# Kernel tuning notes

Hardware: AMD Instinct MI355X
Metric: run time of the kernel (lower is better)

Reference implementation:

```python
import jax, jax.numpy as jnp
import numpy as np
from jax import lax

SOFTPLUS_THRESHOLD = 20.0

def _softplus_thresh(z):
    # softplus(z, beta=1, threshold=20): linear above threshold
    return jnp.where(z > SOFTPLUS_THRESHOLD, z,
                     jnp.log1p(jnp.exp(jnp.minimum(z, SOFTPLUS_THRESHOLD))))

def setup_inputs() -> dict:
    key = jax.random.key(0)
    ks = jax.random.split(key, 8)
    L, E, R, N = 512, 5120, 160, 16
    scale = 0.02
    x = jax.random.normal(ks[0], (1, 1, L, E), dtype=jnp.float32)
    W_dt_low = jax.random.normal(ks[1], (E, R), dtype=jnp.float32) * scale
    W_dt = jax.random.normal(ks[2], (R, E), dtype=jnp.float32) * scale
    dt_bias = jax.random.normal(ks[3], (E,), dtype=jnp.float32) * scale
    W_B = jax.random.normal(ks[4], (E, N), dtype=jnp.float32) * scale
    W_C = jax.random.normal(ks[5], (E, N), dtype=jnp.float32) * scale
    # A_log ~ log of positive values so A = -exp(A_log) is a stable decay
    A_log = jnp.log(1.0 + jax.random.uniform(ks[6], (E, N), dtype=jnp.float32) * 15.0)
    D = jax.random.normal(ks[7], (E,), dtype=jnp.float32)
    return {"x": x, "W_dt_low": W_dt_low, "W_dt": W_dt, "dt_bias": dt_bias,
            "W_B": W_B, "W_C": W_C, "A_log": A_log, "D": D}

def reference(x, W_dt_low, W_dt, dt_bias, W_B, W_C, A_log, D):
    orig_shape = x.shape              # [1,1,L,E]
    L, E = orig_shape[-2], orig_shape[-1]
    xf = x.reshape(L, E)
    # delta_t: x -> dt_rank -> d_inner, then thresholded softplus
    delta = _softplus_thresh((xf @ W_dt_low) @ W_dt + dt_bias)   # [L,E]
    A = -jnp.exp(A_log)                                          # [E,N]
    # discretization: abar = exp(delta * A), bbar = delta * B * x
    abar = jnp.exp(delta[:, :, None] * A[None])                  # [L,E,N]
    B = xf @ W_B                                                 # [L,N]
    bbar = delta[:, :, None] * B[:, None, :] * xf[:, :, None]    # [L,E,N]
    # linear recurrence h_t = abar_t * h_{t-1} + bbar_t via associative scan
    def combine(c1, c2):
        a1, b1 = c1
        a2, b2 = c2
        return a1 * a2, a2 * b1 + b2
    _, h = lax.associative_scan(combine, (abar, bbar), axis=0)   # [L,E,N]
    C = xf @ W_C                                                 # [L,N]
    y = jnp.einsum('len,ln->le', h, C)                           # hc_sum_reduce
    out = xf * D + y
    return out.reshape(orig_shape)
```

## Files before the change

kernel.cpp:

```cpp
#include <hip/hip_runtime.h>
#include <math.h>

#define LL 512
#define EE 5120
#define RR 160
#define NS 16
#define NTOT 192
#define KS 32
#define KCHUNK 160
#define CH 8
#define NC 64

#define XCONV_BLOCKS 1280
#define WALL_TILES   960
#define WDT_TILES    800

typedef __attribute__((ext_vector_type(8))) short short8;
typedef __attribute__((ext_vector_type(4))) short short4v;
typedef __attribute__((ext_vector_type(4))) float f32x4;

__device__ inline float softplus_t(float z) {
    return z > 20.f ? z : log1pf(__expf(fminf(z, 20.f)));
}

__device__ inline short f2bf(float f) {
    unsigned u = __float_as_uint(f);
    unsigned r = (u + 0x7FFFu + ((u >> 16) & 1u)) >> 16;
    return (short)r;
}

__device__ inline float bf2f(unsigned short u) {
    return __uint_as_float(((unsigned)u) << 16);
}

__global__ __launch_bounds__(256) void prep_kernel(
        const float* __restrict__ x,
        const float* __restrict__ Wlow,
        const float* __restrict__ WB,
        const float* __restrict__ WC,
        const float* __restrict__ Wdt,
        short* __restrict__ xb,
        short* __restrict__ WallT,
        short* __restrict__ WdtT) {
    const int tid = threadIdx.x;
    const int bid = blockIdx.x;
    if (bid < XCONV_BLOCKS) {
        size_t base = (size_t)bid * 2048 + (size_t)tid * 8;
        float4 v0 = *reinterpret_cast<const float4*>(x + base);
        float4 v1 = *reinterpret_cast<const float4*>(x + base + 4);
        short8 o;
        o[0] = f2bf(v0.x); o[1] = f2bf(v0.y); o[2] = f2bf(v0.z); o[3] = f2bf(v0.w);
        o[4] = f2bf(v1.x); o[5] = f2bf(v1.y); o[6] = f2bf(v1.z); o[7] = f2bf(v1.w);
        *reinterpret_cast<short8*>(xb + base) = o;
        return;
    }
    __shared__ float tile[32][33];
    const int row = tid >> 3, col4 = (tid & 7) * 4;
    if (bid < XCONV_BLOCKS + WALL_TILES) {
        const int t = bid - XCONV_BLOCKS;
        const int k0 = (t / 6) * 32, n0 = (t % 6) * 32;
#pragma unroll
        for (int i = 0; i < 4; ++i) {
            int n = n0 + col4 + i, k = k0 + row;
            float v;
            if (n < RR)            v = Wlow[(size_t)k * RR + n];
            else if (n < RR + NS)  v = WB[(size_t)k * NS + (n - RR)];
            else                   v = WC[(size_t)k * NS + (n - RR - NS)];
            tile[row][col4 + i] = v;
        }
        __syncthreads();
        const int nr = tid >> 3, kc = (tid & 7) * 4;
        short4v o;
#pragma unroll
        for (int i = 0; i < 4; ++i) o[i] = f2bf(tile[kc + i][nr]);
        *reinterpret_cast<short4v*>(WallT + (size_t)(n0 + nr) * EE + k0 + kc) = o;
    } else {
        const int t = bid - XCONV_BLOCKS - WALL_TILES;
        const int n0 = (t / 5) * 32, k0 = (t % 5) * 32;
#pragma unroll
        for (int i = 0; i < 4; ++i)
            tile[row][col4 + i] = Wdt[(size_t)(k0 + row) * EE + n0 + col4 + i];
        __syncthreads();
        const int nr = tid >> 3, kc = (tid & 7) * 4;
        short4v o;
#pragma unroll
        for (int i = 0; i < 4; ++i) o[i] = f2bf(tile[kc + i][nr]);
        *reinterpret_cast<short4v*>(WdtT + (size_t)(n0 + nr) * RR + k0 + kc) = o;
    }
}

__global__ __launch_bounds__(256) void g1m_kernel(
        const short* __restrict__ xb,
        const short* __restrict__ WallT,
        short* __restrict__ part) {
    const int tid = threadIdx.x;
    const int w = tid >> 6, l = tid & 63;
    const int wm = w >> 1, wn = w & 1;
    const int m0 = blockIdx.x * 64 + wm * 32;
    const int n0 = blockIdx.y * 64 + wn * 32;
    const int kz = blockIdx.z;
    const int row16 = l & 15, kg = (l >> 4) * 8;
    f32x4 acc[2][2] = {};
    const short* ap0 = xb + (size_t)(m0 + row16) * EE + kz * KCHUNK + kg;
    const short* ap1 = ap0 + (size_t)16 * EE;
    const short* bp0 = WallT + (size_t)(n0 + row16) * EE + kz * KCHUNK + kg;
    const short* bp1 = bp0 + (size_t)16 * EE;
#pragma unroll
    for (int s = 0; s < KCHUNK / 32; ++s) {
        short8 a0 = *reinterpret_cast<const short8*>(ap0 + s * 32);
        short8 a1 = *reinterpret_cast<const short8*>(ap1 + s * 32);
        short8 b0 = *reinterpret_cast<const short8*>(bp0 + s * 32);
        short8 b1 = *reinterpret_cast<const short8*>(bp1 + s * 32);
        acc[0][0] = __builtin_amdgcn_mfma_f32_16x16x32_bf16(a0, b0, acc[0][0], 0, 0, 0);
        acc[0][1] = __builtin_amdgcn_mfma_f32_16x16x32_bf16(a0, b1, acc[0][1], 0, 0, 0);
        acc[1][0] = __builtin_amdgcn_mfma_f32_16x16x32_bf16(a1, b0, acc[1][0], 0, 0, 0);
        acc[1][1] = __builtin_amdgcn_mfma_f32_16x16x32_bf16(a1, b1, acc[1][1], 0, 0, 0);
    }
    const int r0 = (l >> 4) * 4;
    const int c = l & 15;
#pragma unroll
    for (int i = 0; i < 2; ++i)
#pragma unroll
        for (int j = 0; j < 2; ++j) {
            size_t base = ((size_t)kz * LL + (m0 + i * 16 + r0)) * NTOT + (n0 + j * 16 + c);
            part[base]            = f2bf(acc[i][j][0]);
            part[base + NTOT]     = f2bf(acc[i][j][1]);
            part[base + 2 * NTOT] = f2bf(acc[i][j][2]);
            part[base + 3 * NTOT] = f2bf(acc[i][j][3]);
        }
}

__global__ __launch_bounds__(256) void r1_kernel(
        const short* __restrict__ part,
        short* __restrict__ tmpb,
        float* __restrict__ Bb,
        float* __restrict__ Cb) {
    int idx = blockIdx.x * 256 + threadIdx.x;
    int m = idx / NTOT, j = idx % NTOT;
    float s = 0.f;
#pragma unroll
    for (int ks = 0; ks < KS; ++ks)
        s += bf2f((unsigned short)part[(size_t)ks * LL * NTOT + idx]);
    if (j < RR) tmpb[m * RR + j] = f2bf(s);
    else if (j < RR + NS) Bb[m * NS + (j - RR)] = s;
    else Cb[m * NS + (j - RR - NS)] = s;
}

__global__ __launch_bounds__(256) void g2m_kernel(
        const short* __restrict__ tmpb,
        const short* __restrict__ WdtT,
        const float* __restrict__ bias,
        unsigned short* __restrict__ deltab) {
    const int tid = threadIdx.x;
    const int w = tid >> 6, l = tid & 63;
    const int wm = w >> 1, wn = w & 1;
    const int m0 = blockIdx.x * 64 + wm * 32;
    const int n0 = blockIdx.y * 64 + wn * 32;
    const int row16 = l & 15, koff = (l >> 4) * 8;
    f32x4 acc[2][2] = {};
    const short* aptr0 = tmpb + (size_t)(m0 + row16) * RR + koff;
    const short* aptr1 = aptr0 + (size_t)16 * RR;
    const short* bptr0 = WdtT + (size_t)(n0 + row16) * RR + koff;
    const short* bptr1 = bptr0 + (size_t)16 * RR;
#pragma unroll
    for (int s = 0; s < 5; ++s) {
        short8 a0 = *reinterpret_cast<const short8*>(aptr0 + s * 32);
        short8 a1 = *reinterpret_cast<const short8*>(aptr1 + s * 32);
        short8 b0 = *reinterpret_cast<const short8*>(bptr0 + s * 32);
        short8 b1 = *reinterpret_cast<const short8*>(bptr1 + s * 32);
        acc[0][0] = __builtin_amdgcn_mfma_f32_16x16x32_bf16(a0, b0, acc[0][0], 0, 0, 0);
        acc[0][1] = __builtin_amdgcn_mfma_f32_16x16x32_bf16(a0, b1, acc[0][1], 0, 0, 0);
        acc[1][0] = __builtin_amdgcn_mfma_f32_16x16x32_bf16(a1, b0, acc[1][0], 0, 0, 0);
        acc[1][1] = __builtin_amdgcn_mfma_f32_16x16x32_bf16(a1, b1, acc[1][1], 0, 0, 0);
    }
    const int r0 = (l >> 4) * 4;
    const int c = l & 15;
#pragma unroll
    for (int i = 0; i < 2; ++i) {
        int m = m0 + i * 16 + r0;
#pragma unroll
        for (int j = 0; j < 2; ++j) {
            int n = n0 + j * 16 + c;
            float bv = bias[n];
#pragma unroll
            for (int r = 0; r < 4; ++r)
                deltab[(size_t)(m + r) * EE + n] =
                    (unsigned short)f2bf(softplus_t(acc[i][j][r] + bv));
        }
    }
}

__global__ __launch_bounds__(256) void passA_kernel(
        const unsigned short* __restrict__ deltab,
        const unsigned short* __restrict__ xb,
        const float* __restrict__ Bb,
        const float* __restrict__ A_log,
        unsigned short* __restrict__ Hloc,
        float* __restrict__ sumd) {
    __shared__ float b_lds[CH][NS];
    const int c = blockIdx.y;
    const int e = blockIdx.x * 256 + threadIdx.x;
    const int t0 = c * CH;
    for (int v = threadIdx.x; v < CH * NS; v += 256)
        b_lds[v >> 4][v & 15] = Bb[t0 * NS + v];
    __syncthreads();

    float Ac[NS];
#pragma unroll
    for (int q = 0; q < 4; ++q) {
        float4 al = *reinterpret_cast<const float4*>(&A_log[(size_t)e * NS + q * 4]);
        Ac[q * 4 + 0] = -__expf(al.x);
        Ac[q * 4 + 1] = -__expf(al.y);
        Ac[q * 4 + 2] = -__expf(al.z);
        Ac[q * 4 + 3] = -__expf(al.w);
    }
    float h[NS];
#pragma unroll
    for (int n = 0; n < NS; ++n) h[n] = 0.f;
    float sd = 0.f;

#pragma unroll
    for (int tt = 0; tt < CH; ++tt) {
        float d  = bf2f(deltab[(size_t)(t0 + tt) * EE + e]);
        float xv = bf2f(xb[(size_t)(t0 + tt) * EE + e]);
        sd += d;
        float bx = d * xv;
#pragma unroll
        for (int n = 0; n < NS; ++n) {
            float a = __expf(d * Ac[n]);
            h[n] = a * h[n] + bx * b_lds[tt][n];
        }
    }
    size_t base = ((size_t)c * EE + e) * NS;
    short8 p0, p1;
#pragma unroll
    for (int n = 0; n < 8; ++n) { p0[n] = f2bf(h[n]); p1[n] = f2bf(h[n + 8]); }
    *reinterpret_cast<short8*>(Hloc + base)     = p0;
    *reinterpret_cast<short8*>(Hloc + base + 8) = p1;
    sumd[(size_t)c * EE + e] = sd;
}

__global__ __launch_bounds__(256) void passB_kernel(
        const unsigned short* __restrict__ Hloc,
        const float* __restrict__ sumd,
        const float* __restrict__ A_log,
        unsigned short* __restrict__ Hstart) {
    const int wk = blockIdx.x * 256 + threadIdx.x;
    const int eB = wk >> 4;
    const float AcB = -__expf(A_log[wk]);
    float hs = 0.f;
#pragma unroll
    for (int cc = 0; cc < NC; ++cc) {
        size_t off = (size_t)cc * EE * NS + wk;
        Hstart[off] = (unsigned short)f2bf(hs);
        hs = __expf(AcB * sumd[(size_t)cc * EE + eB]) * hs + bf2f(Hloc[off]);
    }
}

__global__ __launch_bounds__(256) void passC_kernel(
        const unsigned short* __restrict__ deltab,
        const unsigned short* __restrict__ xb,
        const float* __restrict__ Bb,
        const float* __restrict__ Cb,
        const float* __restrict__ A_log,
        const float* __restrict__ Dvec,
        const unsigned short* __restrict__ Hstart,
        float* __restrict__ out) {
    __shared__ float b_lds[CH][NS];
    __shared__ float c_lds[CH][NS];
    const int c = blockIdx.y;
    const int e = blockIdx.x * 256 + threadIdx.x;
    const int t0 = c * CH;
    for (int v = threadIdx.x; v < CH * NS; v += 256) {
        b_lds[v >> 4][v & 15] = Bb[t0 * NS + v];
        c_lds[v >> 4][v & 15] = Cb[t0 * NS + v];
    }
    __syncthreads();

    float Ac[NS];
#pragma unroll
    for (int q = 0; q < 4; ++q) {
        float4 al = *reinterpret_cast<const float4*>(&A_log[(size_t)e * NS + q * 4]);
        Ac[q * 4 + 0] = -__expf(al.x);
        Ac[q * 4 + 1] = -__expf(al.y);
        Ac[q * 4 + 2] = -__expf(al.z);
        Ac[q * 4 + 3] = -__expf(al.w);
    }
    float h[NS];
    size_t base = ((size_t)c * EE + e) * NS;
    {
        short8 p0 = *reinterpret_cast<const short8*>(Hstart + base);
        short8 p1 = *reinterpret_cast<const short8*>(Hstart + base + 8);
#pragma unroll
        for (int n = 0; n < 8; ++n) {
            h[n]     = bf2f((unsigned short)p0[n]);
            h[n + 8] = bf2f((unsigned short)p1[n]);
        }
    }
    const float Dval = Dvec[e];

#pragma unroll
    for (int tt = 0; tt < CH; ++tt) {
        float d  = bf2f(deltab[(size_t)(t0 + tt) * EE + e]);
        float xv = bf2f(xb[(size_t)(t0 + tt) * EE + e]);
        float bx = d * xv;
        float y = 0.f;
#pragma unroll
        for (int n = 0; n < NS; ++n) {
            float a = __expf(d * Ac[n]);
            h[n] = a * h[n] + bx * b_lds[tt][n];
            y += h[n] * c_lds[tt][n];
        }
        out[(size_t)(t0 + tt) * EE + e] = xv * Dval + y;
    }
}

extern "C" void kernel_launch(void* const* d_in, const int* in_sizes, int n_in,
                              void* d_out, int out_size, void* d_ws, size_t ws_size,
                              hipStream_t stream) {
    const float* x     = (const float*)d_in[0];
    const float* Wlow  = (const float*)d_in[1];
    const float* Wdt   = (const float*)d_in[2];
    const float* bias  = (const float*)d_in[3];
    const float* WB    = (const float*)d_in[4];
    const float* WC    = (const float*)d_in[5];
    const float* Alog  = (const float*)d_in[6];
    const float* Dv    = (const float*)d_in[7];
    float* out = (float*)d_out;
    float* wsf = (float*)d_ws;

    float*          Bb     = wsf;
    float*          Cb     = wsf + 8192;
    short*          WallT  = (short*)(wsf + 16384);
    short*          WdtT   = (short*)(wsf + 507904);
    short*          tmpb   = (short*)(wsf + 917504);
    short*          xb     = (short*)(wsf + 958464);
    short*          part   = (short*)(wsf + 2269184);
    unsigned short* deltab = (unsigned short*)(wsf + 3842048);
    unsigned short* Hloc   = (unsigned short*)(wsf + 5152768);
    unsigned short* Hstart = (unsigned short*)(wsf + 7774208);
    float*          sumd   = wsf + 10395648;

    prep_kernel<<<dim3(XCONV_BLOCKS + WALL_TILES + WDT_TILES), 256, 0, stream>>>(
        x, Wlow, WB, WC, Wdt, xb, WallT, WdtT);
    g1m_kernel<<<dim3(8, 3, KS), 256, 0, stream>>>(xb, WallT, part);
    r1_kernel<<<dim3(384), 256, 0, stream>>>(part, tmpb, Bb, Cb);
    g2m_kernel<<<dim3(8, 80), 256, 0, stream>>>(tmpb, WdtT, bias, deltab);
    passA_kernel<<<dim3(EE / 256, NC), 256, 0, stream>>>(
        deltab, (const unsigned short*)xb, Bb, Alog, Hloc, sumd);
    passB_kernel<<<dim3((EE * NS) / 256), 256, 0, stream>>>(Hloc, sumd, Alog, Hstart);
    passC_kernel<<<dim3(EE / 256, NC), 256, 0, stream>>>(
        deltab, (const unsigned short*)xb, Bb, Cb, Alog, Dv, Hstart, out);
}
```

Measured before the change: 70.77 us.

## Fold inter-chunk carry scan into passC and double chunk length

Removes the separate passB kernel, which turned per-chunk local states into chunk start states. Each passC block now rebuilds its own start state by scanning all earlier chunks' local states and delta sums. The chunk length doubles and the chunk count halves, which keeps that redundant prefix work down. In exchange, later chunks do O(c) extra loads and exps, the work is unevenly spread across blocks, and each chunk runs a longer serial recurrence.

Result: slower. 76.61 us (+8.2%).

```diff
diff --git a/kernel.cpp b/kernel.cpp
--- a/kernel.cpp
+++ b/kernel.cpp
@@ -8,8 +8,8 @@
 #define NTOT 192
 #define KS 32
 #define KCHUNK 160
-#define CH 8
-#define NC 64
+#define CH 16
+#define NC 32
 
 #define XCONV_BLOCKS 1280
 #define WALL_TILES   960
@@ -240,23 +240,6 @@
     sumd[(size_t)c * EE + e] = sd;
 }
 
-__global__ __launch_bounds__(256) void passB_kernel(
-        const unsigned short* __restrict__ Hloc,
-        const float* __restrict__ sumd,
-        const float* __restrict__ A_log,
-        unsigned short* __restrict__ Hstart) {
-    const int wk = blockIdx.x * 256 + threadIdx.x;
-    const int eB = wk >> 4;
-    const float AcB = -__expf(A_log[wk]);
-    float hs = 0.f;
-#pragma unroll
-    for (int cc = 0; cc < NC; ++cc) {
-        size_t off = (size_t)cc * EE * NS + wk;
-        Hstart[off] = (unsigned short)f2bf(hs);
-        hs = __expf(AcB * sumd[(size_t)cc * EE + eB]) * hs + bf2f(Hloc[off]);
-    }
-}
-
 __global__ __launch_bounds__(256) void passC_kernel(
         const unsigned short* __restrict__ deltab,
         const unsigned short* __restrict__ xb,
@@ -264,7 +247,8 @@
         const float* __restrict__ Cb,
         const float* __restrict__ A_log,
         const float* __restrict__ Dvec,
-        const unsigned short* __restrict__ Hstart,
+        const unsigned short* __restrict__ Hloc,
+        const float* __restrict__ sumd,
         float* __restrict__ out) {
     __shared__ float b_lds[CH][NS];
     __shared__ float c_lds[CH][NS];
@@ -286,19 +270,24 @@
         Ac[q * 4 + 2] = -__expf(al.z);
         Ac[q * 4 + 3] = -__expf(al.w);
     }
+
     float h[NS];
-    size_t base = ((size_t)c * EE + e) * NS;
-    {
-        short8 p0 = *reinterpret_cast<const short8*>(Hstart + base);
-        short8 p1 = *reinterpret_cast<const short8*>(Hstart + base + 8);
+#pragma unroll
+    for (int n = 0; n < NS; ++n) h[n] = 0.f;
+#pragma unroll 4
+    for (int cc = 0; cc < c; ++cc) {
+        float sdc = sumd[(size_t)cc * EE + e];
+        size_t off = ((size_t)cc * EE + e) * NS;
+        short8 p0 = *reinterpret_cast<const short8*>(Hloc + off);
+        short8 p1 = *reinterpret_cast<const short8*>(Hloc + off + 8);
 #pragma unroll
         for (int n = 0; n < 8; ++n) {
-            h[n]     = bf2f((unsigned short)p0[n]);
-            h[n + 8] = bf2f((unsigned short)p1[n]);
-        }
-    }
+            h[n]     = __expf(Ac[n] * sdc)     * h[n]     + bf2f((unsigned short)p0[n]);
+            h[n + 8] = __expf(Ac[n + 8] * sdc) * h[n + 8] + bf2f((unsigned short)p1[n]);
+        }
+    }
+
     const float Dval = Dvec[e];
-
 #pragma unroll
     for (int tt = 0; tt < CH; ++tt) {
         float d  = bf2f(deltab[(size_t)(t0 + tt) * EE + e]);
@@ -338,8 +327,7 @@
     short*          part   = (short*)(wsf + 2269184);
     unsigned short* deltab = (unsigned short*)(wsf + 3842048);
     unsigned short* Hloc   = (unsigned short*)(wsf + 5152768);
-    unsigned short* Hstart = (unsigned short*)(wsf + 7774208);
-    float*          sumd   = wsf + 10395648;
+    float*          sumd   = wsf + 6463488;
 
     prep_kernel<<<dim3(XCONV_BLOCKS + WALL_TILES + WDT_TILES), 256, 0, stream>>>(
         x, Wlow, WB, WC, Wdt, xb, WallT, WdtT);
@@ -348,7 +336,6 @@
     g2m_kernel<<<dim3(8, 80), 256, 0, stream>>>(tmpb, WdtT, bias, deltab);
     passA_kernel<<<dim3(EE / 256, NC), 256, 0, stream>>>(
         deltab, (const unsigned short*)xb, Bb, Alog, Hloc, sumd);
-    passB_kernel<<<dim3((EE * NS) / 256), 256, 0, stream>>>(Hloc, sumd, Alog, Hstart);
     passC_kernel<<<dim3(EE / 256, NC), 256, 0, stream>>>(
-        deltab, (const unsigned short*)xb, Bb, Cb, Alog, Dv, Hstart, out);
-}
+        deltab, (const unsigned short*)xb, Bb, Cb, Alog, Dv, Hloc, sumd, out);
+}
```

## Compute local scan output in pass A and correct with carry-in in pass C

Applied to the files above, without the earlier changes.

Pass A now runs the local chunk scan once, emitting the zero-initialised local output y and the cumulative delta per timestep alongside chunk-end states. Pass C no longer redoes the recurrence. It adds the carry-in contribution C·(Hstart·exp(A·cumd)) over finer 8-step tiles, giving more parallelism. The chunk size doubles to 16 and the exps switch to exp2f with prescaled A. This trades a second full recurrence for extra bf16 traffic (y and cumd), and adds bf16 rounding of the cumulative delta, which may affect accuracy.

New measurement: 79.08 us. 1.12x slower.

```diff
diff --git a/kernel.cpp b/kernel.cpp
--- a/kernel.cpp
+++ b/kernel.cpp
@@ -8,12 +8,15 @@
 #define NTOT 192
 #define KS 32
 #define KCHUNK 160
-#define CH 8
-#define NC 64
+#define CH 16
+#define NC 32
+#define TRC 8
 
 #define XCONV_BLOCKS 1280
 #define WALL_TILES   960
 #define WDT_TILES    800
+
+#define LOG2E 1.4426950408889634f
 
 typedef __attribute__((ext_vector_type(8))) short short8;
 typedef __attribute__((ext_vector_type(4))) short short4v;
@@ -194,78 +197,12 @@
         const unsigned short* __restrict__ deltab,
         const unsigned short* __restrict__ xb,
         const float* __restrict__ Bb,
+        const float* __restrict__ Cb,
         const float* __restrict__ A_log,
         unsigned short* __restrict__ Hloc,
-        float* __restrict__ sumd) {
-    __shared__ float b_lds[CH][NS];
-    const int c = blockIdx.y;
-    const int e = blockIdx.x * 256 + threadIdx.x;
-    const int t0 = c * CH;
-    for (int v = threadIdx.x; v < CH * NS; v += 256)
-        b_lds[v >> 4][v & 15] = Bb[t0 * NS + v];
-    __syncthreads();
-
-    float Ac[NS];
-#pragma unroll
-    for (int q = 0; q < 4; ++q) {
-        float4 al = *reinterpret_cast<const float4*>(&A_log[(size_t)e * NS + q * 4]);
-        Ac[q * 4 + 0] = -__expf(al.x);
-        Ac[q * 4 + 1] = -__expf(al.y);
-        Ac[q * 4 + 2] = -__expf(al.z);
-        Ac[q * 4 + 3] = -__expf(al.w);
-    }
-    float h[NS];
-#pragma unroll
-    for (int n = 0; n < NS; ++n) h[n] = 0.f;
-    float sd = 0.f;
-
-#pragma unroll
-    for (int tt = 0; tt < CH; ++tt) {
-        float d  = bf2f(deltab[(size_t)(t0 + tt) * EE + e]);
-        float xv = bf2f(xb[(size_t)(t0 + tt) * EE + e]);
-        sd += d;
-        float bx = d * xv;
-#pragma unroll
-        for (int n = 0; n < NS; ++n) {
-            float a = __expf(d * Ac[n]);
-            h[n] = a * h[n] + bx * b_lds[tt][n];
-        }
-    }
-    size_t base = ((size_t)c * EE + e) * NS;
-    short8 p0, p1;
-#pragma unroll
-    for (int n = 0; n < 8; ++n) { p0[n] = f2bf(h[n]); p1[n] = f2bf(h[n + 8]); }
-    *reinterpret_cast<short8*>(Hloc + base)     = p0;
-    *reinterpret_cast<short8*>(Hloc + base + 8) = p1;
-    sumd[(size_t)c * EE + e] = sd;
-}
-
-__global__ __launch_bounds__(256) void passB_kernel(
-        const unsigned short* __restrict__ Hloc,
-        const float* __restrict__ sumd,
-        const float* __restrict__ A_log,
-        unsigned short* __restrict__ Hstart) {
-    const int wk = blockIdx.x * 256 + threadIdx.x;
-    const int eB = wk >> 4;
-    const float AcB = -__expf(A_log[wk]);
-    float hs = 0.f;
-#pragma unroll
-    for (int cc = 0; cc < NC; ++cc) {
-        size_t off = (size_t)cc * EE * NS + wk;
-        Hstart[off] = (unsigned short)f2bf(hs);
-        hs = __expf(AcB * sumd[(size_t)cc * EE + eB]) * hs + bf2f(Hloc[off]);
-    }
-}
-
-__global__ __launch_bounds__(256) void passC_kernel(
-        const unsigned short* __restrict__ deltab,
-        const unsigned short* __restrict__ xb,
-        const float* __restrict__ Bb,
-        const float* __restrict__ Cb,
-        const float* __restrict__ A_log,
-        const float* __restrict__ Dvec,
-        const unsigned short* __restrict__ Hstart,
-        float* __restrict__ out) {
+        float* __restrict__ sumd,
+        unsigned short* __restrict__ ylocb,
+        unsigned short* __restrict__ cumdb) {
     __shared__ float b_lds[CH][NS];
     __shared__ float c_lds[CH][NS];
     const int c = blockIdx.y;
@@ -277,41 +214,111 @@
     }
     __syncthreads();
 
-    float Ac[NS];
+    float Ac2[NS];
 #pragma unroll
     for (int q = 0; q < 4; ++q) {
         float4 al = *reinterpret_cast<const float4*>(&A_log[(size_t)e * NS + q * 4]);
-        Ac[q * 4 + 0] = -__expf(al.x);
-        Ac[q * 4 + 1] = -__expf(al.y);
-        Ac[q * 4 + 2] = -__expf(al.z);
-        Ac[q * 4 + 3] = -__expf(al.w);
+        Ac2[q * 4 + 0] = -__expf(al.x) * LOG2E;
+        Ac2[q * 4 + 1] = -__expf(al.y) * LOG2E;
+        Ac2[q * 4 + 2] = -__expf(al.z) * LOG2E;
+        Ac2[q * 4 + 3] = -__expf(al.w) * LOG2E;
     }
     float h[NS];
-    size_t base = ((size_t)c * EE + e) * NS;
-    {
-        short8 p0 = *reinterpret_cast<const short8*>(Hstart + base);
-        short8 p1 = *reinterpret_cast<const short8*>(Hstart + base + 8);
-#pragma unroll
-        for (int n = 0; n < 8; ++n) {
-            h[n]     = bf2f((unsigned short)p0[n]);
-            h[n + 8] = bf2f((unsigned short)p1[n]);
-        }
-    }
-    const float Dval = Dvec[e];
+#pragma unroll
+    for (int n = 0; n < NS; ++n) h[n] = 0.f;
+    float sd = 0.f;
 
 #pragma unroll
     for (int tt = 0; tt < CH; ++tt) {
         float d  = bf2f(deltab[(size_t)(t0 + tt) * EE + e]);
         float xv = bf2f(xb[(size_t)(t0 + tt) * EE + e]);
+        sd += d;
         float bx = d * xv;
-        float y = 0.f;
+        float yv = 0.f;
 #pragma unroll
         for (int n = 0; n < NS; ++n) {
-            float a = __expf(d * Ac[n]);
+            float a = exp2f(d * Ac2[n]);
             h[n] = a * h[n] + bx * b_lds[tt][n];
-            y += h[n] * c_lds[tt][n];
-        }
-        out[(size_t)(t0 + tt) * EE + e] = xv * Dval + y;
+            yv += h[n] * c_lds[tt][n];
+        }
+        ylocb[(size_t)(t0 + tt) * EE + e] = (unsigned short)f2bf(yv);
+        cumdb[(size_t)(t0 + tt) * EE + e] = (unsigned short)f2bf(sd);
+    }
+    size_t base = ((size_t)c * EE + e) * NS;
+    short8 p0, p1;
+#pragma unroll
+    for (int n = 0; n < 8; ++n) { p0[n] = f2bf(h[n]); p1[n] = f2bf(h[n + 8]); }
+    *reinterpret_cast<short8*>(Hloc + base)     = p0;
+    *reinterpret_cast<short8*>(Hloc + base + 8) = p1;
+    sumd[(size_t)c * EE + e] = sd;
+}
+
+__global__ __launch_bounds__(256) void passB_kernel(
+        const unsigned short* __restrict__ Hloc,
+        const float* __restrict__ sumd,
+        const float* __restrict__ A_log,
+        unsigned short* __restrict__ Hstart) {
+    const int wk = blockIdx.x * 256 + threadIdx.x;
+    const int eB = wk >> 4;
+    const float Ac2B = -__expf(A_log[wk]) * LOG2E;
+    float hs = 0.f;
+#pragma unroll
+    for (int cc = 0; cc < NC; ++cc) {
+        size_t off = (size_t)cc * EE * NS + wk;
+        Hstart[off] = (unsigned short)f2bf(hs);
+        hs = exp2f(Ac2B * sumd[(size_t)cc * EE + eB]) * hs + bf2f(Hloc[off]);
+    }
+}
+
+__global__ __launch_bounds__(256) void passC_kernel(
+        const unsigned short* __restrict__ ylocb,
+        const unsigned short* __restrict__ cumdb,
+        const unsigned short* __restrict__ xb,
+        const float* __restrict__ Cb,
+        const float* __restrict__ A_log,
+        const float* __restrict__ Dvec,
+        const unsigned short* __restrict__ Hstart,
+        float* __restrict__ out) {
+    __shared__ float c_lds[TRC][NS];
+    const int tb = blockIdx.y * TRC;
+    const int c = tb / CH;
+    const int e = blockIdx.x * 256 + threadIdx.x;
+    if (threadIdx.x < TRC * NS)
+        c_lds[threadIdx.x >> 4][threadIdx.x & 15] = Cb[tb * NS + threadIdx.x];
+    __syncthreads();
+
+    float Ac2[NS];
+#pragma unroll
+    for (int q = 0; q < 4; ++q) {
+        float4 al = *reinterpret_cast<const float4*>(&A_log[(size_t)e * NS + q * 4]);
+        Ac2[q * 4 + 0] = -__expf(al.x) * LOG2E;
+        Ac2[q * 4 + 1] = -__expf(al.y) * LOG2E;
+        Ac2[q * 4 + 2] = -__expf(al.z) * LOG2E;
+        Ac2[q * 4 + 3] = -__expf(al.w) * LOG2E;
+    }
+    float Hs[NS];
+    {
+        size_t base = ((size_t)c * EE + e) * NS;
+        short8 p0 = *reinterpret_cast<const short8*>(Hstart + base);
+        short8 p1 = *reinterpret_cast<const short8*>(Hstart + base + 8);
+#pragma unroll
+        for (int n = 0; n < 8; ++n) {
+            Hs[n]     = bf2f((unsigned short)p0[n]);
+            Hs[n + 8] = bf2f((unsigned short)p1[n]);
+        }
+    }
+    const float Dval = Dvec[e];
+
+#pragma unroll
+    for (int tt = 0; tt < TRC; ++tt) {
+        size_t idx = (size_t)(tb + tt) * EE + e;
+        float y  = bf2f(ylocb[idx]);
+        float cd = bf2f(cumdb[idx]);
+        float xv = bf2f(xb[idx]);
+#pragma unroll
+        for (int n = 0; n < NS; ++n)
+            y += c_lds[tt][n] * (Hs[n] * exp2f(cd * Ac2[n]));
+        out[idx] = xv * Dval + y;
     }
 }
 
@@ -338,7 +345,9 @@
     short*          part   = (short*)(wsf + 2269184);
     unsigned short* deltab = (unsigned short*)(wsf + 3842048);
     unsigned short* Hloc   = (unsigned short*)(wsf + 5152768);
-    unsigned short* Hstart = (unsigned short*)(wsf + 7774208);
+    unsigned short* Hstart = (unsigned short*)(wsf + 6463488);
+    unsigned short* ylocb  = (unsigned short*)(wsf + 7774208);
+    unsigned short* cumdb  = (unsigned short*)(wsf + 9084928);
     float*          sumd   = wsf + 10395648;
 
     prep_kernel<<<dim3(XCONV_BLOCKS + WALL_TILES + WDT_TILES), 256, 0, stream>>>(
@@ -347,8 +356,8 @@
     r1_kernel<<<dim3(384), 256, 0, stream>>>(part, tmpb, Bb, Cb);
     g2m_kernel<<<dim3(8, 80), 256, 0, stream>>>(tmpb, WdtT, bias, deltab);
     passA_kernel<<<dim3(EE / 256, NC), 256, 0, stream>>>(
-        deltab, (const unsigned short*)xb, Bb, Alog, Hloc, sumd);
+        deltab, (const unsigned short*)xb, Bb, Cb, Alog, Hloc, sumd, ylocb, cumdb);
     passB_kernel<<<dim3((EE * NS) / 256), 256, 0, stream>>>(Hloc, sumd, Alog, Hstart);
-    passC_kernel<<<dim3(EE / 256, NC), 256, 0, stream>>>(
-        deltab, (const unsigned short*)xb, Bb, Cb, Alog, Dv, Hstart, out);
-}
+    passC_kernel<<<dim3(EE / 256, LL / TRC), 256, 0, stream>>>(
+        ylocb, cumdb, (const unsigned short*)xb, Cb, Alog, Dv, Hstart, out);
+}
```

## Transpose delta and x to time-contiguous layout, double scan chunk length

Applied to the files above, without the earlier changes.

The prep kernel now also writes a transposed bf16 copy of x, and the delta GEMM writes its output transposed (E-major), so each scan thread can load its 16 time steps with vector loads instead of strided per-step loads. The chunk length doubles to 16 with half as many chunks, which halves the Hloc/Hstart state traffic and the serial passB length. The exp calls in the scans switch to exp2f with a log2e-prescaled A. In exchange the transposed stores in prep and g2m are strided, scan parallelism is halved, and the extra xbT buffer is added.

New measurement: 82.16 us. +16.1%, slower.

```diff
diff --git a/kernel.cpp b/kernel.cpp
--- a/kernel.cpp
+++ b/kernel.cpp
@@ -8,12 +8,14 @@
 #define NTOT 192
 #define KS 32
 #define KCHUNK 160
-#define CH 8
-#define NC 64
-
-#define XCONV_BLOCKS 1280
+#define CH 16
+#define NC 32
+
+#define XT_TILES     2560
 #define WALL_TILES   960
 #define WDT_TILES    800
+
+#define LOG2E 1.4426950408889634f
 
 typedef __attribute__((ext_vector_type(8))) short short8;
 typedef __attribute__((ext_vector_type(4))) short short4v;
@@ -40,24 +42,32 @@
         const float* __restrict__ WC,
         const float* __restrict__ Wdt,
         short* __restrict__ xb,
+        short* __restrict__ xbT,
         short* __restrict__ WallT,
         short* __restrict__ WdtT) {
     const int tid = threadIdx.x;
     const int bid = blockIdx.x;
-    if (bid < XCONV_BLOCKS) {
-        size_t base = (size_t)bid * 2048 + (size_t)tid * 8;
-        float4 v0 = *reinterpret_cast<const float4*>(x + base);
-        float4 v1 = *reinterpret_cast<const float4*>(x + base + 4);
-        short8 o;
-        o[0] = f2bf(v0.x); o[1] = f2bf(v0.y); o[2] = f2bf(v0.z); o[3] = f2bf(v0.w);
-        o[4] = f2bf(v1.x); o[5] = f2bf(v1.y); o[6] = f2bf(v1.z); o[7] = f2bf(v1.w);
-        *reinterpret_cast<short8*>(xb + base) = o;
-        return;
-    }
     __shared__ float tile[32][33];
     const int row = tid >> 3, col4 = (tid & 7) * 4;
-    if (bid < XCONV_BLOCKS + WALL_TILES) {
-        const int t = bid - XCONV_BLOCKS;
+    if (bid < XT_TILES) {
+        const int t0 = (bid / 160) * 32;
+        const int e0 = (bid % 160) * 32;
+        short4v s;
+#pragma unroll
+        for (int i = 0; i < 4; ++i) {
+            float v = x[(size_t)(t0 + row) * EE + e0 + col4 + i];
+            tile[row][col4 + i] = v;
+            s[i] = f2bf(v);
+        }
+        *reinterpret_cast<short4v*>(xb + (size_t)(t0 + row) * EE + e0 + col4) = s;
+        __syncthreads();
+        const int nr = tid >> 3, kc = (tid & 7) * 4;
+        short4v o;
+#pragma unroll
+        for (int i = 0; i < 4; ++i) o[i] = f2bf(tile[kc + i][nr]);
+        *reinterpret_cast<short4v*>(xbT + (size_t)(e0 + nr) * LL + t0 + kc) = o;
+    } else if (bid < XT_TILES + WALL_TILES) {
+        const int t = bid - XT_TILES;
         const int k0 = (t / 6) * 32, n0 = (t % 6) * 32;
 #pragma unroll
         for (int i = 0; i < 4; ++i) {
@@ -75,7 +85,7 @@
         for (int i = 0; i < 4; ++i) o[i] = f2bf(tile[kc + i][nr]);
         *reinterpret_cast<short4v*>(WallT + (size_t)(n0 + nr) * EE + k0 + kc) = o;
     } else {
-        const int t = bid - XCONV_BLOCKS - WALL_TILES;
+        const int t = bid - XT_TILES - WALL_TILES;
         const int n0 = (t / 5) * 32, k0 = (t % 5) * 32;
 #pragma unroll
         for (int i = 0; i < 4; ++i)
@@ -146,28 +156,28 @@
     else Cb[m * NS + (j - RR - NS)] = s;
 }
 
-__global__ __launch_bounds__(256) void g2m_kernel(
+__global__ __launch_bounds__(256) void g2mT_kernel(
         const short* __restrict__ tmpb,
         const short* __restrict__ WdtT,
         const float* __restrict__ bias,
-        unsigned short* __restrict__ deltab) {
+        unsigned short* __restrict__ deltaT) {
     const int tid = threadIdx.x;
     const int w = tid >> 6, l = tid & 63;
-    const int wm = w >> 1, wn = w & 1;
-    const int m0 = blockIdx.x * 64 + wm * 32;
-    const int n0 = blockIdx.y * 64 + wn * 32;
+    const int we = w >> 1, wt = w & 1;
+    const int e0 = blockIdx.y * 64 + we * 32;
+    const int t0 = blockIdx.x * 64 + wt * 32;
     const int row16 = l & 15, koff = (l >> 4) * 8;
     f32x4 acc[2][2] = {};
-    const short* aptr0 = tmpb + (size_t)(m0 + row16) * RR + koff;
-    const short* aptr1 = aptr0 + (size_t)16 * RR;
-    const short* bptr0 = WdtT + (size_t)(n0 + row16) * RR + koff;
-    const short* bptr1 = bptr0 + (size_t)16 * RR;
+    const short* ap0 = WdtT + (size_t)(e0 + row16) * RR + koff;
+    const short* ap1 = ap0 + (size_t)16 * RR;
+    const short* bp0 = tmpb + (size_t)(t0 + row16) * RR + koff;
+    const short* bp1 = bp0 + (size_t)16 * RR;
 #pragma unroll
     for (int s = 0; s < 5; ++s) {
-        short8 a0 = *reinterpret_cast<const short8*>(aptr0 + s * 32);
-        short8 a1 = *reinterpret_cast<const short8*>(aptr1 + s * 32);
-        short8 b0 = *reinterpret_cast<const short8*>(bptr0 + s * 32);
-        short8 b1 = *reinterpret_cast<const short8*>(bptr1 + s * 32);
+        short8 a0 = *reinterpret_cast<const short8*>(ap0 + s * 32);
+        short8 a1 = *reinterpret_cast<const short8*>(ap1 + s * 32);
+        short8 b0 = *reinterpret_cast<const short8*>(bp0 + s * 32);
+        short8 b1 = *reinterpret_cast<const short8*>(bp1 + s * 32);
         acc[0][0] = __builtin_amdgcn_mfma_f32_16x16x32_bf16(a0, b0, acc[0][0], 0, 0, 0);
         acc[0][1] = __builtin_amdgcn_mfma_f32_16x16x32_bf16(a0, b1, acc[0][1], 0, 0, 0);
         acc[1][0] = __builtin_amdgcn_mfma_f32_16x16x32_bf16(a1, b0, acc[1][0], 0, 0, 0);
@@ -177,22 +187,24 @@
     const int c = l & 15;
 #pragma unroll
     for (int i = 0; i < 2; ++i) {
-        int m = m0 + i * 16 + r0;
+        float4 bv = *reinterpret_cast<const float4*>(&bias[e0 + i * 16 + r0]);
 #pragma unroll
         for (int j = 0; j < 2; ++j) {
-            int n = n0 + j * 16 + c;
-            float bv = bias[n];
-#pragma unroll
-            for (int r = 0; r < 4; ++r)
-                deltab[(size_t)(m + r) * EE + n] =
-                    (unsigned short)f2bf(softplus_t(acc[i][j][r] + bv));
+            int t = t0 + j * 16 + c;
+#pragma unroll
+            for (int r = 0; r < 4; ++r) {
+                int e = e0 + i * 16 + r0 + r;
+                float b4 = r == 0 ? bv.x : (r == 1 ? bv.y : (r == 2 ? bv.z : bv.w));
+                deltaT[(size_t)e * LL + t] =
+                    (unsigned short)f2bf(softplus_t(acc[i][j][r] + b4));
+            }
         }
     }
 }
 
 __global__ __launch_bounds__(256) void passA_kernel(
-        const unsigned short* __restrict__ deltab,
-        const unsigned short* __restrict__ xb,
+        const unsigned short* __restrict__ deltaT,
+        const unsigned short* __restrict__ xbT,
         const float* __restrict__ Bb,
         const float* __restrict__ A_log,
         unsigned short* __restrict__ Hloc,
@@ -205,14 +217,26 @@
         b_lds[v >> 4][v & 15] = Bb[t0 * NS + v];
     __syncthreads();
 
-    float Ac[NS];
+    float Ac2[NS];
 #pragma unroll
     for (int q = 0; q < 4; ++q) {
         float4 al = *reinterpret_cast<const float4*>(&A_log[(size_t)e * NS + q * 4]);
-        Ac[q * 4 + 0] = -__expf(al.x);
-        Ac[q * 4 + 1] = -__expf(al.y);
-        Ac[q * 4 + 2] = -__expf(al.z);
-        Ac[q * 4 + 3] = -__expf(al.w);
+        Ac2[q * 4 + 0] = -__expf(al.x) * LOG2E;
+        Ac2[q * 4 + 1] = -__expf(al.y) * LOG2E;
+        Ac2[q * 4 + 2] = -__expf(al.z) * LOG2E;
+        Ac2[q * 4 + 3] = -__expf(al.w) * LOG2E;
+    }
+    float dv[CH], xv[CH];
+    {
+        short8 d0 = *reinterpret_cast<const short8*>(deltaT + (size_t)e * LL + t0);
+        short8 d1 = *reinterpret_cast<const short8*>(deltaT + (size_t)e * LL + t0 + 8);
+        short8 x0 = *reinterpret_cast<const short8*>(xbT + (size_t)e * LL + t0);
+        short8 x1 = *reinterpret_cast<const short8*>(xbT + (size_t)e * LL + t0 + 8);
+#pragma unroll
+        for (int k = 0; k < 8; ++k) {
+            dv[k] = bf2f((unsigned short)d0[k]); dv[k + 8] = bf2f((unsigned short)d1[k]);
+            xv[k] = bf2f((unsigned short)x0[k]); xv[k + 8] = bf2f((unsigned short)x1[k]);
+        }
     }
     float h[NS];
 #pragma unroll
@@ -221,13 +245,12 @@
 
 #pragma unroll
     for (int tt = 0; tt < CH; ++tt) {
-        float d  = bf2f(deltab[(size_t)(t0 + tt) * EE + e]);
-        float xv = bf2f(xb[(size_t)(t0 + tt) * EE + e]);
+        float d = dv[tt];
         sd += d;
-        float bx = d * xv;
+        float bx = d * xv[tt];
 #pragma unroll
         for (int n = 0; n < NS; ++n) {
-            float a = __expf(d * Ac[n]);
+            float a = exp2f(d * Ac2[n]);
             h[n] = a * h[n] + bx * b_lds[tt][n];
         }
     }
@@ -247,19 +270,19 @@
         unsigned short* __restrict__ Hstart) {
     const int wk = blockIdx.x * 256 + threadIdx.x;
     const int eB = wk >> 4;
-    const float AcB = -__expf(A_log[wk]);
+    const float Ac2B = -__expf(A_log[wk]) * LOG2E;
     float hs = 0.f;
 #pragma unroll
     for (int cc = 0; cc < NC; ++cc) {
         size_t off = (size_t)cc * EE * NS + wk;
         Hstart[off] = (unsigned short)f2bf(hs);
-        hs = __expf(AcB * sumd[(size_t)cc * EE + eB]) * hs + bf2f(Hloc[off]);
+        hs = exp2f(Ac2B * sumd[(size_t)cc * EE + eB]) * hs + bf2f(Hloc[off]);
     }
 }
 
 __global__ __launch_bounds__(256) void passC_kernel(
-        const unsigned short* __restrict__ deltab,
-        const unsigned short* __restrict__ xb,
+        const unsigned short* __restrict__ deltaT,
+        const unsigned short* __restrict__ xbT,
         const float* __restrict__ Bb,
         const float* __restrict__ Cb,
         const float* __restrict__ A_log,
@@ -277,14 +300,26 @@
     }
     __syncthreads();
 
-    float Ac[NS];
+    float Ac2[NS];
 #pragma unroll
     for (int q = 0; q < 4; ++q) {
         float4 al = *reinterpret_cast<const float4*>(&A_log[(size_t)e * NS + q * 4]);
-        Ac[q * 4 + 0] = -__expf(al.x);
-        Ac[q * 4 + 1] = -__expf(al.y);
-        Ac[q * 4 + 2] = -__expf(al.z);
-        Ac[q * 4 + 3] = -__expf(al.w);
+        Ac2[q * 4 + 0] = -__expf(al.x) * LOG2E;
+        Ac2[q * 4 + 1] = -__expf(al.y) * LOG2E;
+        Ac2[q * 4 + 2] = -__expf(al.z) * LOG2E;
+        Ac2[q * 4 + 3] = -__expf(al.w) * LOG2E;
+    }
+    float dv[CH], xv[CH];
+    {
+        short8 d0 = *reinterpret_cast<const short8*>(deltaT + (size_t)e * LL + t0);
+        short8 d1 = *reinterpret_cast<const short8*>(deltaT + (size_t)e * LL + t0 + 8);
+        short8 x0 = *reinterpret_cast<const short8*>(xbT + (size_t)e * LL + t0);
+        short8 x1 = *reinterpret_cast<const short8*>(xbT + (size_t)e * LL + t0 + 8);
+#pragma unroll
+        for (int k = 0; k < 8; ++k) {
+            dv[k] = bf2f((unsigned short)d0[k]); dv[k + 8] = bf2f((unsigned short)d1[k]);
+            xv[k] = bf2f((unsigned short)x0[k]); xv[k + 8] = bf2f((unsigned short)x1[k]);
+        }
     }
     float h[NS];
     size_t base = ((size_t)c * EE + e) * NS;
@@ -301,17 +336,16 @@
 
 #pragma unroll
     for (int tt = 0; tt < CH; ++tt) {
-        float d  = bf2f(deltab[(size_t)(t0 + tt) * EE + e]);
-        float xv = bf2f(xb[(size_t)(t0 + tt) * EE + e]);
-        float bx = d * xv;
+        float d = dv[tt];
+        float bx = d * xv[tt];
         float y = 0.f;
 #pragma unroll
         for (int n = 0; n < NS; ++n) {
-            float a = __expf(d * Ac[n]);
+            float a = exp2f(d * Ac2[n]);
             h[n] = a * h[n] + bx * b_lds[tt][n];
             y += h[n] * c_lds[tt][n];
         }
-        out[(size_t)(t0 + tt) * EE + e] = xv * Dval + y;
+        out[(size_t)(t0 + tt) * EE + e] = xv[tt] * Dval + y;
     }
 }
 
@@ -335,20 +369,21 @@
     short*          WdtT   = (short*)(wsf + 507904);
     short*          tmpb   = (short*)(wsf + 917504);
     short*          xb     = (short*)(wsf + 958464);
-    short*          part   = (short*)(wsf + 2269184);
-    unsigned short* deltab = (unsigned short*)(wsf + 3842048);
-    unsigned short* Hloc   = (unsigned short*)(wsf + 5152768);
+    short*          xbT    = (short*)(wsf + 2269184);
+    short*          part   = (short*)(wsf + 3579904);
+    unsigned short* deltaT = (unsigned short*)(wsf + 5152768);
+    unsigned short* Hloc   = (unsigned short*)(wsf + 6463488);
     unsigned short* Hstart = (unsigned short*)(wsf + 7774208);
-    float*          sumd   = wsf + 10395648;
-
-    prep_kernel<<<dim3(XCONV_BLOCKS + WALL_TILES + WDT_TILES), 256, 0, stream>>>(
-        x, Wlow, WB, WC, Wdt, xb, WallT, WdtT);
+    float*          sumd   = wsf + 9084928;
+
+    prep_kernel<<<dim3(XT_TILES + WALL_TILES + WDT_TILES), 256, 0, stream>>>(
+        x, Wlow, WB, WC, Wdt, xb, xbT, WallT, WdtT);
     g1m_kernel<<<dim3(8, 3, KS), 256, 0, stream>>>(xb, WallT, part);
     r1_kernel<<<dim3(384), 256, 0, stream>>>(part, tmpb, Bb, Cb);
-    g2m_kernel<<<dim3(8, 80), 256, 0, stream>>>(tmpb, WdtT, bias, deltab);
+    g2mT_kernel<<<dim3(8, 80), 256, 0, stream>>>(tmpb, WdtT, bias, deltaT);
     passA_kernel<<<dim3(EE / 256, NC), 256, 0, stream>>>(
-        deltab, (const unsigned short*)xb, Bb, Alog, Hloc, sumd);
+        deltaT, (const unsigned short*)xbT, Bb, Alog, Hloc, sumd);
     passB_kernel<<<dim3((EE * NS) / 256), 256, 0, stream>>>(Hloc, sumd, Alog, Hstart);
     passC_kernel<<<dim3(EE / 256, NC), 256, 0, stream>>>(
-        deltab, (const unsigned short*)xb, Bb, Cb, Alog, Dv, Hstart, out);
-}
+        deltaT, (const unsigned short*)xbT, Bb, Cb, Alog, Dv, Hstart, out);
+}
```
